# Kernel optimization log

Measured on AMD Instinct MI355X. Metric: run time of the kernel, lower is better.

Reference implementation:

```python
import jax, jax.numpy as jnp
import numpy as np

_DIMS = [("fu1",2,2),("fu2",2,2),("ku1",4,4),("ku2",4,4),("hu1",6,6),("hu2",6,6),("md1",11,16),("md2",16,16),("md3",16,6),("hd1",6,4),("hd2",4,4),("kd1",4,2),("kd2",2,2),("ha1",8,4),("ha2",4,1),("ka1",6,4),("ka2",4,1),("fa1",4,4),("fa2",4,1)]


def setup_inputs() -> dict:
    key = jax.random.key(0)
    B = 2_000_000
    inp = {"x": jax.random.normal(key, (B, 11), dtype=jnp.float32)}
    for i, (name, din, dout) in enumerate(_DIMS):
        kw = jax.random.fold_in(key, i + 1)
        scale = float(np.sqrt(6.0 / (din + dout)))  # xavier_uniform gain=1
        inp[name + "_w"] = jax.random.uniform(kw, (din, dout), jnp.float32, -scale, scale)
        inp[name + "_b"] = jnp.zeros((dout,), jnp.float32)  # nn.Linear default bias ~ small; zeros for determinism
    return inp


def _lin(x, w, b):
    # weights stored as (in, out) == torch W.T
    return x @ w + b


def reference(x, fu1_w, fu1_b, fu2_w, fu2_b, ku1_w, ku1_b, ku2_w, ku2_b, hu1_w, hu1_b, hu2_w, hu2_b, md1_w, md1_b, md2_w, md2_b, md3_w, md3_b, hd1_w, hd1_b, hd2_w, hd2_b, kd1_w, kd1_b, kd2_w, kd2_b, ha1_w, ha1_b, ha2_w, ha2_b, ka1_w, ka1_b, ka2_w, ka2_b, fa1_w, fa1_b, fa2_w, fa2_b):
    r = jax.nn.relu
    h = x[:, 2:3]; k = x[:, 3:4]; f = x[:, 4:5]
    hd = x[:, 8:9]; kd = x[:, 9:10]; fd = x[:, 10:11]
    m_obs = x[:, jnp.array([0, 1, 5, 6, 7])]  # [B,5]
    f_up = r(_lin(r(_lin(jnp.concatenate([f, fd], 1), fu1_w, fu1_b)), fu2_w, fu2_b))            # [B,2]
    k_up = r(_lin(r(_lin(jnp.concatenate([k, kd, f_up], 1), ku1_w, ku1_b)), ku2_w, ku2_b))      # [B,4]
    h_up = r(_lin(r(_lin(jnp.concatenate([h, hd, k_up], 1), hu1_w, hu1_b)), hu2_w, hu2_b))      # [B,6]
    m_in = jnp.concatenate([m_obs, h_up], 1)                                                    # [B,11]
    m_down = r(_lin(r(_lin(r(_lin(m_in, md1_w, md1_b)), md2_w, md2_b)), md3_w, md3_b))          # [B,6]
    h_down = r(_lin(r(_lin(m_down, hd1_w, hd1_b)), hd2_w, hd2_b))                               # [B,4]
    k_down = r(_lin(r(_lin(h_down, kd1_w, kd1_b)), kd2_w, kd2_b))                               # [B,2]
    h_act = _lin(r(_lin(jnp.concatenate([h, hd, m_down], 1), ha1_w, ha1_b)), ha2_w, ha2_b)      # [B,1]
    k_act = _lin(r(_lin(jnp.concatenate([k, kd, h_down], 1), ka1_w, ka1_b)), ka2_w, ka2_b)      # [B,1]
    f_act = _lin(r(_lin(jnp.concatenate([f, fd, k_down], 1), fa1_w, fa1_b)), fa2_w, fa2_b)      # [B,1]
    return jnp.concatenate([h_act, f_act, k_act], 1)                                            # [B,3]
```

## Files before the change

kernel.cpp:

```cpp
#include <hip/hip_runtime.h>

#define BLOCK 256

typedef float v2f __attribute__((ext_vector_type(2)));

struct WPtrs {
    const float* w[19];
    const float* b[19];
};

struct WDup {
    const v2f* w[19];
    const v2f* b[19];
};

enum LId {FU1,FU2,KU1,KU2,HU1,HU2,MD1,MD2,MD3,HD1,HD2,KD1,KD2,HA1,HA2,KA1,KA2,FA1,FA2};

__constant__ const int kWN[19] = {4,4,16,16,36,36,176,256,96,24,16,8,4,32,4,24,4,16,4};
__constant__ const int kBN[19] = {2,2,4,4,6,6,16,16,6,4,4,2,2,4,1,4,1,4,1};

__global__ void prep_kernel(WPtrs P, float* __restrict__ ws) {
    const int t = threadIdx.x;
    float* dst = ws;
    for (int l = 0; l < 19; ++l) {
        const int wn = kWN[l];
        for (int i = t; i < wn; i += BLOCK) {
            const float v = P.w[l][i];
            dst[2*i] = v; dst[2*i+1] = v;
        }
        dst += 2*wn;
        const int bn = kBN[l];
        for (int i = t; i < bn; i += BLOCK) {
            const float v = P.b[l][i];
            dst[2*i] = v; dst[2*i+1] = v;
        }
        dst += 2*bn;
    }
}

template<int DIN,int DOUT,bool RELU>
__device__ __forceinline__ void lin2(const v2f (&in)[DIN], v2f (&out)[DOUT],
                                     const v2f* __restrict__ wd, const v2f* __restrict__ bd) {
#pragma unroll
    for (int j = 0; j < DOUT; ++j) {
        v2f acc = bd[j];
#pragma unroll
        for (int i = 0; i < DIN; ++i)
            acc = __builtin_elementwise_fma(in[i], wd[i*DOUT + j], acc);
        if (RELU) {
            const v2f z = {0.0f, 0.0f};
            acc = __builtin_elementwise_max(acc, z);
        }
        out[j] = acc;
    }
}

__global__ __launch_bounds__(BLOCK) void pnet_kernel(
    const float* __restrict__ x, float* __restrict__ out, int B, WDup P) {
    const int tid  = threadIdx.x;
    const int rowA = blockIdx.x * (BLOCK * 2) + tid;
    const int rowB = rowA + BLOCK;

    const int rA = rowA < B ? rowA : (B - 1);
    const int rB = rowB < B ? rowB : (B - 1);
    const float* pA = x + (long long)rA * 11;
    const float* pB = x + (long long)rB * 11;
    v2f xin[11];
#pragma unroll
    for (int c = 0; c < 11; ++c) { xin[c].x = pA[c]; xin[c].y = pB[c]; }

    v2f fin[2] = {xin[4], xin[10]};
    v2f tf[2], f_up[2];
    lin2<2,2,true>(fin, tf, P.w[FU1], P.b[FU1]);
    lin2<2,2,true>(tf, f_up, P.w[FU2], P.b[FU2]);

    v2f kin[4] = {xin[3], xin[9], f_up[0], f_up[1]};
    v2f tk[4], k_up[4];
    lin2<4,4,true>(kin, tk, P.w[KU1], P.b[KU1]);
    lin2<4,4,true>(tk, k_up, P.w[KU2], P.b[KU2]);

    v2f hin[6] = {xin[2], xin[8], k_up[0], k_up[1], k_up[2], k_up[3]};
    v2f th[6], h_up[6];
    lin2<6,6,true>(hin, th, P.w[HU1], P.b[HU1]);
    lin2<6,6,true>(th, h_up, P.w[HU2], P.b[HU2]);

    v2f min_[11] = {xin[0], xin[1], xin[5], xin[6], xin[7],
                    h_up[0], h_up[1], h_up[2], h_up[3], h_up[4], h_up[5]};
    v2f t16a[16], t16b[16], m_down[6];
    lin2<11,16,true>(min_, t16a, P.w[MD1], P.b[MD1]);
    lin2<16,16,true>(t16a, t16b, P.w[MD2], P.b[MD2]);
    lin2<16,6,true>(t16b, m_down, P.w[MD3], P.b[MD3]);

    v2f t4b[4], h_down[4];
    lin2<6,4,true>(m_down, t4b, P.w[HD1], P.b[HD1]);
    lin2<4,4,true>(t4b, h_down, P.w[HD2], P.b[HD2]);

    v2f t2b[2], k_down[2];
    lin2<4,2,true>(h_down, t2b, P.w[KD1], P.b[KD1]);
    lin2<2,2,true>(t2b, k_down, P.w[KD2], P.b[KD2]);

    v2f ha_in[8] = {xin[2], xin[8], m_down[0], m_down[1],
                    m_down[2], m_down[3], m_down[4], m_down[5]};
    v2f t4c[4], h_act[1];
    lin2<8,4,true>(ha_in, t4c, P.w[HA1], P.b[HA1]);
    lin2<4,1,false>(t4c, h_act, P.w[HA2], P.b[HA2]);

    v2f ka_in[6] = {xin[3], xin[9], h_down[0], h_down[1], h_down[2], h_down[3]};
    v2f t4d[4], k_act[1];
    lin2<6,4,true>(ka_in, t4d, P.w[KA1], P.b[KA1]);
    lin2<4,1,false>(t4d, k_act, P.w[KA2], P.b[KA2]);

    v2f fa_in[4] = {xin[4], xin[10], k_down[0], k_down[1]};
    v2f t4e[4], f_act[1];
    lin2<4,4,true>(fa_in, t4e, P.w[FA1], P.b[FA1]);
    lin2<4,1,false>(t4e, f_act, P.w[FA2], P.b[FA2]);

    if (rowA < B) {
        float* po = out + (long long)rowA * 3;
        po[0] = h_act[0].x;
        po[1] = f_act[0].x;
        po[2] = k_act[0].x;
    }
    if (rowB < B) {
        float* po = out + (long long)rowB * 3;
        po[0] = h_act[0].y;
        po[1] = f_act[0].y;
        po[2] = k_act[0].y;
    }
}

extern "C" void kernel_launch(void* const* d_in, const int* in_sizes, int n_in,
                              void* d_out, int out_size, void* d_ws, size_t ws_size,
                              hipStream_t stream) {
    static const int wn[19] = {4,4,16,16,36,36,176,256,96,24,16,8,4,32,4,24,4,16,4};
    static const int bn[19] = {2,2,4,4,6,6,16,16,6,4,4,2,2,4,1,4,1,4,1};

    const float* x = (const float*)d_in[0];
    float* out = (float*)d_out;
    const int B = in_sizes[0] / 11;

    WPtrs P;
    for (int i = 0; i < 19; ++i) {
        P.w[i] = (const float*)d_in[1 + 2*i];
        P.b[i] = (const float*)d_in[2 + 2*i];
    }

    float* ws = (float*)d_ws;
    WDup D;
    int off = 0;
    for (int l = 0; l < 19; ++l) {
        D.w[l] = (const v2f*)(ws + off); off += 2 * wn[l];
        D.b[l] = (const v2f*)(ws + off); off += 2 * bn[l];
    }

    prep_kernel<<<1, BLOCK, 0, stream>>>(P, ws);

    const long long rows_per_block = (long long)BLOCK * 2;
    const int blocks = (int)((B + rows_per_block - 1) / rows_per_block);
    pnet_kernel<<<blocks, BLOCK, 0, stream>>>(x, out, B, D);
}
```

Baseline: 245.2 us.

## Process four rows per thread to reuse weight loads across two packed pairs

Each thread now computes four batch rows as two packed float2 pairs, so every duplicated weight load feeds two packed FMAs instead of one. The goal is to halve weight-fetch traffic per row and raise ILP, and launch bounds request 4 waves' occupancy. The prep kernel is also parallelised with one block per layer. The cost is higher register pressure and half as many blocks, which could limit latency hiding for the memory-bound input loads.

Measured after the change: 345.9 us. +41.1%, slower.

```diff
diff --git a/kernel.cpp b/kernel.cpp
--- a/kernel.cpp
+++ b/kernel.cpp
@@ -20,113 +20,134 @@
 __constant__ const int kBN[19] = {2,2,4,4,6,6,16,16,6,4,4,2,2,4,1,4,1,4,1};
 
 __global__ void prep_kernel(WPtrs P, float* __restrict__ ws) {
+    const int l = blockIdx.x;
     const int t = threadIdx.x;
-    float* dst = ws;
-    for (int l = 0; l < 19; ++l) {
-        const int wn = kWN[l];
-        for (int i = t; i < wn; i += BLOCK) {
-            const float v = P.w[l][i];
-            dst[2*i] = v; dst[2*i+1] = v;
-        }
-        dst += 2*wn;
-        const int bn = kBN[l];
-        for (int i = t; i < bn; i += BLOCK) {
-            const float v = P.b[l][i];
-            dst[2*i] = v; dst[2*i+1] = v;
-        }
-        dst += 2*bn;
+    int off = 0;
+    for (int i = 0; i < l; ++i) off += 2 * (kWN[i] + kBN[i]);
+    float* dw = ws + off;
+    const int wn = kWN[l];
+    for (int i = t; i < wn; i += BLOCK) {
+        const float v = P.w[l][i];
+        dw[2*i] = v; dw[2*i+1] = v;
+    }
+    float* db = dw + 2*wn;
+    const int bn = kBN[l];
+    for (int i = t; i < bn; i += BLOCK) {
+        const float v = P.b[l][i];
+        db[2*i] = v; db[2*i+1] = v;
     }
 }
 
 template<int DIN,int DOUT,bool RELU>
-__device__ __forceinline__ void lin2(const v2f (&in)[DIN], v2f (&out)[DOUT],
+__device__ __forceinline__ void lin4(const v2f (&inA)[DIN], const v2f (&inB)[DIN],
+                                     v2f (&outA)[DOUT], v2f (&outB)[DOUT],
                                      const v2f* __restrict__ wd, const v2f* __restrict__ bd) {
 #pragma unroll
     for (int j = 0; j < DOUT; ++j) {
-        v2f acc = bd[j];
+        v2f accA = bd[j];
+        v2f accB = bd[j];
 #pragma unroll
-        for (int i = 0; i < DIN; ++i)
-            acc = __builtin_elementwise_fma(in[i], wd[i*DOUT + j], acc);
+        for (int i = 0; i < DIN; ++i) {
+            const v2f wv = wd[i*DOUT + j];
+            accA = __builtin_elementwise_fma(inA[i], wv, accA);
+            accB = __builtin_elementwise_fma(inB[i], wv, accB);
+        }
         if (RELU) {
             const v2f z = {0.0f, 0.0f};
-            acc = __builtin_elementwise_max(acc, z);
+            accA = __builtin_elementwise_max(accA, z);
+            accB = __builtin_elementwise_max(accB, z);
         }
-        out[j] = acc;
+        outA[j] = accA;
+        outB[j] = accB;
     }
 }
 
-__global__ __launch_bounds__(BLOCK) void pnet_kernel(
+__global__ __launch_bounds__(BLOCK, 4) void pnet_kernel(
     const float* __restrict__ x, float* __restrict__ out, int B, WDup P) {
-    const int tid  = threadIdx.x;
-    const int rowA = blockIdx.x * (BLOCK * 2) + tid;
-    const int rowB = rowA + BLOCK;
+    const int tid = threadIdx.x;
+    const int r0 = blockIdx.x * (BLOCK * 4) + tid;
+    const int r1 = r0 + BLOCK;
+    const int r2 = r0 + 2*BLOCK;
+    const int r3 = r0 + 3*BLOCK;
 
-    const int rA = rowA < B ? rowA : (B - 1);
-    const int rB = rowB < B ? rowB : (B - 1);
-    const float* pA = x + (long long)rA * 11;
-    const float* pB = x + (long long)rB * 11;
-    v2f xin[11];
+    const int c0 = r0 < B ? r0 : (B - 1);
+    const int c1 = r1 < B ? r1 : (B - 1);
+    const int c2 = r2 < B ? r2 : (B - 1);
+    const int c3 = r3 < B ? r3 : (B - 1);
+    const float* p0 = x + (long long)c0 * 11;
+    const float* p1 = x + (long long)c1 * 11;
+    const float* p2 = x + (long long)c2 * 11;
+    const float* p3 = x + (long long)c3 * 11;
+
+    v2f xinA[11], xinB[11];
 #pragma unroll
-    for (int c = 0; c < 11; ++c) { xin[c].x = pA[c]; xin[c].y = pB[c]; }
+    for (int c = 0; c < 11; ++c) {
+        xinA[c].x = p0[c]; xinA[c].y = p1[c];
+        xinB[c].x = p2[c]; xinB[c].y = p3[c];
+    }
 
-    v2f fin[2] = {xin[4], xin[10]};
-    v2f tf[2], f_up[2];
-    lin2<2,2,true>(fin, tf, P.w[FU1], P.b[FU1]);
-    lin2<2,2,true>(tf, f_up, P.w[FU2], P.b[FU2]);
+    v2f finA[2] = {xinA[4], xinA[10]}, finB[2] = {xinB[4], xinB[10]};
+    v2f tfA[2], tfB[2], f_upA[2], f_upB[2];
+    lin4<2,2,true>(finA, finB, tfA, tfB, P.w[FU1], P.b[FU1]);
+    lin4<2,2,true>(tfA, tfB, f_upA, f_upB, P.w[FU2], P.b[FU2]);
 
-    v2f kin[4] = {xin[3], xin[9], f_up[0], f_up[1]};
-    v2f tk[4], k_up[4];
-    lin2<4,4,true>(kin, tk, P.w[KU1], P.b[KU1]);
-    lin2<4,4,true>(tk, k_up, P.w[KU2], P.b[KU2]);
+    v2f kinA[4] = {xinA[3], xinA[9], f_upA[0], f_upA[1]};
+    v2f kinB[4] = {xinB[3], xinB[9], f_upB[0], f_upB[1]};
+    v2f tkA[4], tkB[4], k_upA[4], k_upB[4];
+    lin4<4,4,true>(kinA, kinB, tkA, tkB, P.w[KU1], P.b[KU1]);
+    lin4<4,4,true>(tkA, tkB, k_upA, k_upB, P.w[KU2], P.b[KU2]);
 
-    v2f hin[6] = {xin[2], xin[8], k_up[0], k_up[1], k_up[2], k_up[3]};
-    v2f th[6], h_up[6];
-    lin2<6,6,true>(hin, th, P.w[HU1], P.b[HU1]);
-    lin2<6,6,true>(th, h_up, P.w[HU2], P.b[HU2]);
+    v2f hinA[6] = {xinA[2], xinA[8], k_upA[0], k_upA[1], k_upA[2], k_upA[3]};
+    v2f hinB[6] = {xinB[2], xinB[8], k_upB[0], k_upB[1], k_upB[2], k_upB[3]};
+    v2f thA[6], thB[6], h_upA[6], h_upB[6];
+    lin4<6,6,true>(hinA, hinB, thA, thB, P.w[HU1], P.b[HU1]);
+    lin4<6,6,true>(thA, thB, h_upA, h_upB, P.w[HU2], P.b[HU2]);
 
-    v2f min_[11] = {xin[0], xin[1], xin[5], xin[6], xin[7],
-                    h_up[0], h_up[1], h_up[2], h_up[3], h_up[4], h_up[5]};
-    v2f t16a[16], t16b[16], m_down[6];
-    lin2<11,16,true>(min_, t16a, P.w[MD1], P.b[MD1]);
-    lin2<16,16,true>(t16a, t16b, P.w[MD2], P.b[MD2]);
-    lin2<16,6,true>(t16b, m_down, P.w[MD3], P.b[MD3]);
+    v2f minA[11] = {xinA[0], xinA[1], xinA[5], xinA[6], xinA[7],
+                    h_upA[0], h_upA[1], h_upA[2], h_upA[3], h_upA[4], h_upA[5]};
+    v2f minB[11] = {xinB[0], xinB[1], xinB[5], xinB[6], xinB[7],
+                    h_upB[0], h_upB[1], h_upB[2], h_upB[3], h_upB[4], h_upB[5]};
+    v2f t16aA[16], t16aB[16], t16bA[16], t16bB[16], m_downA[6], m_downB[6];
+    lin4<11,16,true>(minA, minB, t16aA, t16aB, P.w[MD1], P.b[MD1]);
+    lin4<16,16,true>(t16aA, t16aB, t16bA, t16bB, P.w[MD2], P.b[MD2]);
+    lin4<16,6,true>(t16bA, t16bB, m_downA, m_downB, P.w[MD3], P.b[MD3]);
 
-    v2f t4b[4], h_down[4];
-    lin2<6,4,true>(m_down, t4b, P.w[HD1], P.b[HD1]);
-    lin2<4,4,true>(t4b, h_down, P.w[HD2], P.b[HD2]);
+    v2f t4bA[4], t4bB[4], h_downA[4], h_downB[4];
+    lin4<6,4,true>(m_downA, m_downB, t4bA, t4bB, P.w[HD1], P.b[HD1]);
+    lin4<4,4,true>(t4bA, t4bB, h_downA, h_downB, P.w[HD2], P.b[HD2]);
 
-    v2f t2b[2], k_down[2];
-    lin2<4,2,true>(h_down, t2b, P.w[KD1], P.b[KD1]);
-    lin2<2,2,true>(t2b, k_down, P.w[KD2], P.b[KD2]);
+    v2f t2bA[2], t2bB[2], k_downA[2], k_downB[2];
+    lin4<4,2,true>(h_downA, h_downB, t2bA, t2bB, P.w[KD1], P.b[KD1]);
+    lin4<2,2,true>(t2bA, t2bB, k_downA, k_downB, P.w[KD2], P.b[KD2]);
 
-    v2f ha_in[8] = {xin[2], xin[8], m_down[0], m_down[1],
-                    m_down[2], m_down[3], m_down[4], m_down[5]};
-    v2f t4c[4], h_act[1];
-    lin2<8,4,true>(ha_in, t4c, P.w[HA1], P.b[HA1]);
-    lin2<4,1,false>(t4c, h_act, P.w[HA2], P.b[HA2]);
+    v2f haA[8] = {xinA[2], xinA[8], m_downA[0], m_downA[1],
+                  m_downA[2], m_downA[3], m_downA[4], m_downA[5]};
+    v2f haB[8] = {xinB[2], xinB[8], m_downB[0], m_downB[1],
+                  m_downB[2], m_downB[3], m_downB[4], m_downB[5]};
+    v2f t4cA[4], t4cB[4], h_actA[1], h_actB[1];
+    lin4<8,4,true>(haA, haB, t4cA, t4cB, P.w[HA1], P.b[HA1]);
+    lin4<4,1,false>(t4cA, t4cB, h_actA, h_actB, P.w[HA2], P.b[HA2]);
 
-    v2f ka_in[6] = {xin[3], xin[9], h_down[0], h_down[1], h_down[2], h_down[3]};
-    v2f t4d[4], k_act[1];
-    lin2<6,4,true>(ka_in, t4d, P.w[KA1], P.b[KA1]);
-    lin2<4,1,false>(t4d, k_act, P.w[KA2], P.b[KA2]);
+    v2f kaA[6] = {xinA[3], xinA[9], h_downA[0], h_downA[1], h_downA[2], h_downA[3]};
+    v2f kaB[6] = {xinB[3], xinB[9], h_downB[0], h_downB[1], h_downB[2], h_downB[3]};
+    v2f t4dA[4], t4dB[4], k_actA[1], k_actB[1];
+    lin4<6,4,true>(kaA, kaB, t4dA, t4dB, P.w[KA1], P.b[KA1]);
+    lin4<4,1,false>(t4dA, t4dB, k_actA, k_actB, P.w[KA2], P.b[KA2]);
 
-    v2f fa_in[4] = {xin[4], xin[10], k_down[0], k_down[1]};
-    v2f t4e[4], f_act[1];
-    lin2<4,4,true>(fa_in, t4e, P.w[FA1], P.b[FA1]);
-    lin2<4,1,false>(t4e, f_act, P.w[FA2], P.b[FA2]);
+    v2f faA[4] = {xinA[4], xinA[10], k_downA[0], k_downA[1]};
+    v2f faB[4] = {xinB[4], xinB[10], k_downB[0], k_downB[1]};
+    v2f t4eA[4], t4eB[4], f_actA[1], f_actB[1];
+    lin4<4,4,true>(faA, faB, t4eA, t4eB, P.w[FA1], P.b[FA1]);
+    lin4<4,1,false>(t4eA, t4eB, f_actA, f_actB, P.w[FA2], P.b[FA2]);
 
-    if (rowA < B) {
-        float* po = out + (long long)rowA * 3;
-        po[0] = h_act[0].x;
-        po[1] = f_act[0].x;
-        po[2] = k_act[0].x;
-    }
-    if (rowB < B) {
-        float* po = out + (long long)rowB * 3;
-        po[0] = h_act[0].y;
-        po[1] = f_act[0].y;
-        po[2] = k_act[0].y;
-    }
+    if (r0 < B) { float* po = out + (long long)r0 * 3;
+        po[0] = h_actA[0].x; po[1] = f_actA[0].x; po[2] = k_actA[0].x; }
+    if (r1 < B) { float* po = out + (long long)r1 * 3;
+        po[0] = h_actA[0].y; po[1] = f_actA[0].y; po[2] = k_actA[0].y; }
+    if (r2 < B) { float* po = out + (long long)r2 * 3;
+        po[0] = h_actB[0].x; po[1] = f_actB[0].x; po[2] = k_actB[0].x; }
+    if (r3 < B) { float* po = out + (long long)r3 * 3;
+        po[0] = h_actB[0].y; po[1] = f_actB[0].y; po[2] = k_actB[0].y; }
 }
 
 extern "C" void kernel_launch(void* const* d_in, const int* in_sizes, int n_in,
@@ -153,9 +174,9 @@
         D.b[l] = (const v2f*)(ws + off); off += 2 * bn[l];
     }
 
-    prep_kernel<<<1, BLOCK, 0, stream>>>(P, ws);
+    prep_kernel<<<19, BLOCK, 0, stream>>>(P, ws);
 
-    const long long rows_per_block = (long long)BLOCK * 2;
+    const long long rows_per_block = (long long)BLOCK * 4;
     const int blocks = (int)((B + rows_per_block - 1) / rows_per_block);
     pnet_kernel<<<blocks, BLOCK, 0, stream>>>(x, out, B, D);
 }
```
